# Kernel optimization log

Measured on AMD Instinct MI355X. Metric: run time of the kernel, lower is better.

The kernel has to match this reference:

```python
import jax, jax.numpy as jnp
import numpy as np

# Segmented-polynomial (uniform-1d) configuration
E = 128   # operand_extent (uniform segment extent shared by all 1D operands)
S = 64    # number of segments per operand (all three operands)
P = 256   # number of tensor-product paths
B = 4096  # batch size
N = 8192  # rows of the indexed input table (input 0 uses BATCH_DIM_INDEXED)


def setup_inputs() -> dict:
    key = jax.random.key(0)
    k1, k2, k3, k4, k5 = jax.random.split(key, 5)
    x_table = jax.random.normal(k1, (N, S * E), dtype=jnp.float32)
    y = jax.random.normal(k2, (B, S * E), dtype=jnp.float32)
    path_coeff = jax.random.normal(k3, (P,), dtype=jnp.float32)
    x_idx = jax.random.randint(k4, (B,), 0, N, dtype=jnp.int32)
    path_idx = jax.random.randint(k5, (P, 3), 0, S, dtype=jnp.int32)
    return {
        "x_table": x_table,
        "y": y,
        "path_coeff": path_coeff,
        "x_idx": x_idx,
        "path_idx": path_idx,
    }


def reference(x_table, y, path_coeff, x_idx, path_idx):
    """Uniform-1d segmented tensor product:
    out[b, s3, :] += sum_p c_p * x[b, s1(p), :] * y[b, s2(p), :]
    where x[b] = x_table[x_idx[b]] (indexed input buffer).
    All segments share extent E; coefficients are scalar per path.
    """
    b = y.shape[0]
    xs = x_table[x_idx].reshape(b, S, E)   # gather indexed input -> [B, S, E]
    ys = y.reshape(b, S, E)                # [B, S, E]
    i1, i2, i3 = path_idx[:, 0], path_idx[:, 1], path_idx[:, 2]
    # per-path products, [B, P, E]
    prod = path_coeff[None, :, None] * xs[:, i1, :] * ys[:, i2, :]
    # scatter-add into output segments, [B, S, E]
    out = jnp.zeros((b, S, E), dtype=y.dtype).at[:, i3, :].add(prod)
    return out.reshape(b, S * E)
```

## Files before the change

### kernel.cpp

```cpp
#include <hip/hip_runtime.h>

#define E_EXT 128
#define S_SEG 64
#define P_PATH 256
#define SE 8192


__global__ __launch_bounds__(P_PATH) void build_paths_kernel(
    const float* __restrict__ coeff,
    const int* __restrict__ pidx,
    int* __restrict__ seg_start,
    int4* __restrict__ meta)
{
    __shared__ int i3s[P_PATH];
    __shared__ int cnt[S_SEG];
    __shared__ int base[S_SEG + 1];
    const int t = threadIdx.x;
    const int i1 = pidx[3 * t + 0];
    const int i2 = pidx[3 * t + 1];
    const int i3 = pidx[3 * t + 2];
    i3s[t] = i3;
    __syncthreads();
    int pos = 0;
    for (int q = 0; q < t; ++q) pos += (i3s[q] == i3) ? 1 : 0;
    if (t < S_SEG) {
        int c = 0;
        for (int q = 0; q < P_PATH; ++q) c += (i3s[q] == t) ? 1 : 0;
        cnt[t] = c;
    }
    __syncthreads();
    if (t == 0) {
        int run = 0;
        for (int s = 0; s < S_SEG; ++s) { base[s] = run; run += cnt[s]; }
        base[S_SEG] = run;
    }
    __syncthreads();
    if (t <= S_SEG) seg_start[t] = base[t];
    meta[base[i3] + pos] = make_int4(i1 * (E_EXT / 2), i2 * (E_EXT / 2),
                                     __float_as_int(coeff[t]), i3);
}

__global__ __launch_bounds__(512, 2) void tp_main_kernel(
    const float* __restrict__ x_table,
    const float* __restrict__ y,
    const int* __restrict__ x_idx,
    const int* __restrict__ seg_start,
    const int4* __restrict__ meta,
    float* __restrict__ out)
{
    __shared__ float xs[SE];
    __shared__ float ys[SE];
    __shared__ int4 smeta[P_PATH];
    __shared__ int sstart[S_SEG + 1];
    const int b = blockIdx.x;
    const int t = threadIdx.x;

    const float4* __restrict__ xsrc =
        (const float4*)(x_table + (size_t)x_idx[b] * SE);
    const float4* __restrict__ ysrc = (const float4*)(y + (size_t)b * SE);
    float4* xd = (float4*)xs;
    float4* yd = (float4*)ys;
#pragma unroll
    for (int i = 0; i < SE / 4 / 512; ++i) {
        xd[t + i * 512] = xsrc[t + i * 512];
        yd[t + i * 512] = ysrc[t + i * 512];
    }
    if (t < P_PATH) smeta[t] = meta[t];
    if (t <= S_SEG) sstart[t] = seg_start[t];
    __syncthreads();

    const int w = t >> 6;
    const int l = t & 63;
    const float2* __restrict__ xs2 = (const float2*)xs;
    const float2* __restrict__ ys2 = (const float2*)ys;
    float* __restrict__ orow = out + (size_t)b * SE;

#pragma unroll
    for (int si = 0; si < 8; ++si) {
        const int s3 = w * 8 + si;
        const int js = sstart[s3];
        const int je = sstart[s3 + 1];
        float a0 = 0.f, a1 = 0.f;
        int4 r;
        if (js < je) r = smeta[js];
        for (int j = js; j < je; ++j) {
            const int4 cur = r;
            if (j + 1 < je) r = smeta[j + 1];
            const float c = __int_as_float(cur.z);
            const float2 xv = xs2[cur.x + l];
            const float2 yv = ys2[cur.y + l];
            a0 = fmaf(c * xv.x, yv.x, a0);
            a1 = fmaf(c * xv.y, yv.y, a1);
        }
        ((float2*)(orow + (size_t)s3 * E_EXT))[l] = make_float2(a0, a1);
    }
}

extern "C" void kernel_launch(void* const* d_in, const int* in_sizes, int n_in,
                              void* d_out, int out_size, void* d_ws, size_t ws_size,
                              hipStream_t stream) {
    const float* x_table   = (const float*)d_in[0];
    const float* y         = (const float*)d_in[1];
    const float* path_coef = (const float*)d_in[2];
    const int*   x_idx     = (const int*)d_in[3];
    const int*   path_idx  = (const int*)d_in[4];
    float* out = (float*)d_out;

    int* seg_start = (int*)d_ws;
    int4* meta = (int4*)((char*)d_ws + 1024);

    const int B = in_sizes[3];

    build_paths_kernel<<<1, P_PATH, 0, stream>>>(path_coef, path_idx, seg_start, meta);
    tp_main_kernel<<<B, 512, 0, stream>>>(x_table, y, x_idx, seg_start, meta, out);
}
```

Baseline: 463.2 us.

## Split each batch row across two blocks by half-extent to raise occupancy

Each batch row is now processed by two blocks, each taking one 64-element half of every segment. This halves shared memory per block (to about 36KB) and raises the launch-bounds occupancy hint from 2 to 8, so more blocks can be resident to hide the memory latency of the gather loads. The cost is more blocks, half-width global loads (256B contiguous chunks), scalar rather than float2 LDS access and stores, and duplicated metadata loads per block. The inner loop is no longer unrolled.

Measured after the change: 462.4 us. Within noise of the previous version (-0.2%).

```diff
diff --git a/kernel.cpp b/kernel.cpp
--- a/kernel.cpp
+++ b/kernel.cpp
@@ -1,6 +1,7 @@
 #include <hip/hip_runtime.h>
 
 #define E_EXT 128
+#define EH 64
 #define S_SEG 64
 #define P_PATH 256
 #define SE 8192
@@ -36,11 +37,11 @@
     }
     __syncthreads();
     if (t <= S_SEG) seg_start[t] = base[t];
-    meta[base[i3] + pos] = make_int4(i1 * (E_EXT / 2), i2 * (E_EXT / 2),
+    meta[base[i3] + pos] = make_int4(i1 * EH, i2 * EH,
                                      __float_as_int(coeff[t]), i3);
 }
 
-__global__ __launch_bounds__(512, 2) void tp_main_kernel(
+__global__ __launch_bounds__(512, 8) void tp_main_kernel(
     const float* __restrict__ x_table,
     const float* __restrict__ y,
     const int* __restrict__ x_idx,
@@ -48,22 +49,28 @@
     const int4* __restrict__ meta,
     float* __restrict__ out)
 {
-    __shared__ float xs[SE];
-    __shared__ float ys[SE];
+    __shared__ float xs[S_SEG * EH];
+    __shared__ float ys[S_SEG * EH];
     __shared__ int4 smeta[P_PATH];
     __shared__ int sstart[S_SEG + 1];
-    const int b = blockIdx.x;
-    const int t = threadIdx.x;
+
+    const int bb = blockIdx.x;
+    const int b  = bb >> 1;
+    const int h  = bb & 1;
+    const int t  = threadIdx.x;
 
     const float4* __restrict__ xsrc =
-        (const float4*)(x_table + (size_t)x_idx[b] * SE);
-    const float4* __restrict__ ysrc = (const float4*)(y + (size_t)b * SE);
+        (const float4*)(x_table + (size_t)x_idx[b] * SE) + h * (EH / 4);
+    const float4* __restrict__ ysrc =
+        (const float4*)(y + (size_t)b * SE) + h * (EH / 4);
     float4* xd = (float4*)xs;
     float4* yd = (float4*)ys;
 #pragma unroll
-    for (int i = 0; i < SE / 4 / 512; ++i) {
-        xd[t + i * 512] = xsrc[t + i * 512];
-        yd[t + i * 512] = ysrc[t + i * 512];
+    for (int i = 0; i < 2; ++i) {
+        const int j = t + i * 512;
+        const int g = ((j >> 4) << 5) + (j & 15);
+        xd[j] = xsrc[g];
+        yd[j] = ysrc[g];
     }
     if (t < P_PATH) smeta[t] = meta[t];
     if (t <= S_SEG) sstart[t] = seg_start[t];
@@ -71,28 +78,22 @@
 
     const int w = t >> 6;
     const int l = t & 63;
-    const float2* __restrict__ xs2 = (const float2*)xs;
-    const float2* __restrict__ ys2 = (const float2*)ys;
-    float* __restrict__ orow = out + (size_t)b * SE;
+    float* __restrict__ orow = out + (size_t)b * SE + h * EH;
 
-#pragma unroll
     for (int si = 0; si < 8; ++si) {
         const int s3 = w * 8 + si;
         const int js = sstart[s3];
         const int je = sstart[s3 + 1];
-        float a0 = 0.f, a1 = 0.f;
+        float a = 0.f;
         int4 r;
         if (js < je) r = smeta[js];
         for (int j = js; j < je; ++j) {
             const int4 cur = r;
             if (j + 1 < je) r = smeta[j + 1];
             const float c = __int_as_float(cur.z);
-            const float2 xv = xs2[cur.x + l];
-            const float2 yv = ys2[cur.y + l];
-            a0 = fmaf(c * xv.x, yv.x, a0);
-            a1 = fmaf(c * xv.y, yv.y, a1);
+            a = fmaf(c * xs[cur.x + l], ys[cur.y + l], a);
         }
-        ((float2*)(orow + (size_t)s3 * E_EXT))[l] = make_float2(a0, a1);
+        orow[(size_t)s3 * E_EXT + l] = a;
     }
 }
 
@@ -112,5 +113,5 @@
     const int B = in_sizes[3];
 
     build_paths_kernel<<<1, P_PATH, 0, stream>>>(path_coef, path_idx, seg_start, meta);
-    tp_main_kernel<<<B, 512, 0, stream>>>(x_table, y, x_idx, seg_start, meta, out);
+    tp_main_kernel<<<2 * B, 512, 0, stream>>>(x_table, y, x_idx, seg_start, meta, out);
 }
```
